# Performance work log

Hardware: AMD Instinct MI355X
Metric: run time of the kernel (lower is better)

The kernel has to match this reference:

```python
import jax, jax.numpy as jnp
import numpy as np

PROJ_DIM = 512
HIDDEN_DIM = 1024
OUTPUT_DIM = 32000
BATCH = 256
TRG_LEN = 512


def setup_inputs() -> dict:
    key = jax.random.key(0)
    ks = jax.random.split(key, 10)
    H = PROJ_DIM
    inp = {
        "x": jax.random.normal(ks[0], (BATCH, TRG_LEN, 1), dtype=jnp.float32),
        "hidden": jnp.zeros((1, BATCH, H), dtype=jnp.float32),
        "trg": jax.random.randint(ks[1], (BATCH, TRG_LEN), 0, OUTPUT_DIM),
        # LSTM params (PyTorch layout, gate order i,f,g,o)
        "w_ih": jax.random.normal(ks[2], (4 * H, 1), dtype=jnp.float32) * (1.0 / np.sqrt(H)),
        "w_hh": jax.random.normal(ks[3], (4 * H, H), dtype=jnp.float32) * (1.0 / np.sqrt(H)),
        "b_ih": jax.random.normal(ks[4], (4 * H,), dtype=jnp.float32) * 0.01,
        "b_hh": jax.random.normal(ks[5], (4 * H,), dtype=jnp.float32) * 0.01,
        "fc1_w": jax.random.normal(ks[6], (HIDDEN_DIM, H), dtype=jnp.float32) * (1.0 / np.sqrt(H)),
        "fc1_b": jnp.zeros((HIDDEN_DIM,), dtype=jnp.float32),
        "fc2_w": jax.random.normal(ks[7], (OUTPUT_DIM, HIDDEN_DIM), dtype=jnp.float32) * (1.0 / np.sqrt(HIDDEN_DIM)),
        "fc2_b": jnp.zeros((OUTPUT_DIM,), dtype=jnp.float32),
    }
    return inp


def reference(x, hidden, trg, w_ih, w_hh, b_ih, b_hh, fc1_w, fc1_b, fc2_w, fc2_b):
    # hidden arg is ignored (source overwrites it with None). Teacher forcing
    # fixed to True: the fed-back argmax never affects LSTM state, and the
    # return value is only the output at the final timestep.
    B, T = trg.shape
    H = w_hh.shape[1]
    bias = b_ih + b_hh  # (4H,)
    # inputs fed at steps t=1..T-1 are trg[:, 0..T-2] as float scalars
    inputs = trg[:, : T - 1].astype(jnp.float32).T[..., None]  # (T-1, B, 1)

    def step(carry, x_t):
        h, c = carry  # (B, H) each
        gates = x_t @ w_ih.T + h @ w_hh.T + bias  # (B, 4H)
        i, f, g, o = jnp.split(gates, 4, axis=-1)
        i = jax.nn.sigmoid(i)
        f = jax.nn.sigmoid(f)
        g = jnp.tanh(g)
        o = jax.nn.sigmoid(o)
        c = f * c + i * g
        h = o * jnp.tanh(c)
        return (h, c), None

    h0 = jnp.zeros((B, H), dtype=jnp.float32)
    c0 = jnp.zeros((B, H), dtype=jnp.float32)
    (h_last, _), _ = jax.lax.scan(step, (h0, c0), inputs)

    # head applied to final timestep's LSTM output: fc2(relu(fc1(h)))
    z = jax.nn.relu(h_last @ fc1_w.T + fc1_b)  # (B, hidden_dim)
    out = z @ fc2_w.T + fc2_b  # (B, output_dim)
    return out
```

## Files before the change

kernel.cpp:

```cpp
#include <hip/hip_runtime.h>
#include <stdint.h>

typedef uint32_t u32;
typedef uint16_t u16;
typedef __attribute__((ext_vector_type(8))) short bf16x8;
typedef __attribute__((ext_vector_type(4))) float f32x4;

__device__ __forceinline__ u16 f2bf(float f) {
  u32 u = __builtin_bit_cast(u32, f);
  return (u16)((u + 0x7FFFu + ((u >> 16) & 1u)) >> 16);
}
__device__ __forceinline__ u32 pack2bf(float a, float b) {
  return (u32)f2bf(a) | ((u32)f2bf(b) << 16);
}
__device__ __forceinline__ uint4 pack8bf(float4 a, float4 b) {
  uint4 r;
  r.x = pack2bf(a.x, a.y); r.y = pack2bf(a.z, a.w);
  r.z = pack2bf(b.x, b.y); r.w = pack2bf(b.z, b.w);
  return r;
}
__device__ __forceinline__ float sigmoid_(float x) { return 1.0f / (1.0f + __expf(-x)); }
__device__ __forceinline__ float tanh_(float x) { return 1.0f - 2.0f / (1.0f + __expf(2.0f * x)); }

__device__ __forceinline__ void store_h_l3(u16* p, u32 v) {
  asm volatile("global_store_short %0, %1, off sc0 sc1" :: "v"(p), "v"(v) : "memory");
}
__device__ __forceinline__ u32 load_flag_l3(const int* p) {
  u32 v;
  asm volatile("global_load_dword %0, %1, off sc0 sc1\n\ts_waitcnt vmcnt(0)"
               : "=v"(v) : "v"(p) : "memory");
  return v;
}

__global__ __launch_bounds__(256, 2) void lstm_kernel(
    const int* __restrict__ trg, const float* __restrict__ w_ih,
    const float* __restrict__ w_hh, const float* __restrict__ b_ih,
    const float* __restrict__ b_hh, u16* __restrict__ h_buf,
    int* __restrict__ flags) {
  __shared__ u16 Bb[16 * 520];
  __shared__ float Xl[16 * 513];
  const int tid = threadIdx.x;
  const int wave = tid >> 6, lane = tid & 63;
  const int q = lane >> 4, n = lane & 15;
  const int bg = blockIdx.x & 15, ug = blockIdx.x >> 4;

  #pragma unroll
  for (int c = 0; c < 4; ++c) {
    int e = c * 2048 + tid * 8;
    int rn = e >> 9, t0 = e & 511;
    const int* src = trg + (bg * 16 + rn) * 512 + t0;
    int4 a = *(const int4*)src;
    int4 b = *(const int4*)(src + 4);
    float* dst = &Xl[rn * 513 + t0];
    dst[0] = (float)a.x; dst[1] = (float)a.y; dst[2] = (float)a.z; dst[3] = (float)a.w;
    dst[4] = (float)b.x; dst[5] = (float)b.y; dst[6] = (float)b.z; dst[7] = (float)b.w;
  }

  bf16x8 Areg[2][16];
  const int rit = lane & 15;
  #pragma unroll
  for (int i = 0; i < 2; ++i) {
    int tile = wave * 2 + i;
    int grow = (rit & 3) * 512 + ug * 32 + tile * 4 + (rit >> 2);
    const float* wr = w_hh + (size_t)grow * 512;
    #pragma unroll
    for (int ks = 0; ks < 16; ++ks) {
      const float* p = wr + ks * 32 + q * 8;
      float4 f0 = *(const float4*)p;
      float4 f1 = *(const float4*)(p + 4);
      Areg[i][ks] = __builtin_bit_cast(bf16x8, pack8bf(f0, f1));
    }
  }

  float wi[2][4], bs[2][4];
  #pragma unroll
  for (int i = 0; i < 2; ++i) {
    int tile = wave * 2 + i;
    #pragma unroll
    for (int r = 0; r < 4; ++r) {
      int grow = r * 512 + ug * 32 + tile * 4 + q;
      wi[i][r] = w_ih[grow];
      bs[i][r] = b_ih[grow] + b_hh[grow];
    }
  }
  float cst[2] = {0.f, 0.f};
  __syncthreads();

  for (int t = 1; t <= 511; ++t) {
    if (t > 1) {
      const int* fp = &flags[(t - 1) * 16 + bg];
      int cnt = 0;
      u32 v;
      do {
        v = load_flag_l3(fp);
        if (++cnt > (1 << 20)) break;
      } while (v < 16u);
    }
    {
      const u16* src = h_buf + (size_t)(((t - 1) & 1) * 16 + bg) * 8192;
      const u16* p0 = src + 0 * 2048 + tid * 8;
      const u16* p1 = src + 1 * 2048 + tid * 8;
      const u16* p2 = src + 2 * 2048 + tid * 8;
      const u16* p3 = src + 3 * 2048 + tid * 8;
      uint4 d0, d1, d2, d3;
      asm volatile(
          "global_load_dwordx4 %0, %4, off sc0 sc1\n\t"
          "global_load_dwordx4 %1, %5, off sc0 sc1\n\t"
          "global_load_dwordx4 %2, %6, off sc0 sc1\n\t"
          "global_load_dwordx4 %3, %7, off sc0 sc1\n\t"
          "s_waitcnt vmcnt(0)"
          : "=&v"(d0), "=&v"(d1), "=&v"(d2), "=&v"(d3)
          : "v"(p0), "v"(p1), "v"(p2), "v"(p3)
          : "memory");
      #pragma unroll
      for (int c = 0; c < 4; ++c) {
        int e = c * 2048 + tid * 8;
        int rn = e >> 9, k = e & 511;
        uint4 d = (c == 0) ? d0 : (c == 1) ? d1 : (c == 2) ? d2 : d3;
        *(uint4*)&Bb[rn * 520 + k] = d;
      }
    }
    __syncthreads();

    f32x4 acc[2] = {{0.f, 0.f, 0.f, 0.f}, {0.f, 0.f, 0.f, 0.f}};
    const u16* brow = &Bb[n * 520];
    #pragma unroll
    for (int ks = 0; ks < 16; ++ks) {
      bf16x8 bf = *(const bf16x8*)(brow + ks * 32 + q * 8);
      acc[0] = __builtin_amdgcn_mfma_f32_16x16x32_bf16(Areg[0][ks], bf, acc[0], 0, 0, 0);
      acc[1] = __builtin_amdgcn_mfma_f32_16x16x32_bf16(Areg[1][ks], bf, acc[1], 0, 0, 0);
    }

    float x = Xl[n * 513 + (t - 1)];
    u16* hdst = h_buf + (size_t)((t & 1) * 16 + bg) * 8192 + n * 512 + ug * 32 + q;
    #pragma unroll
    for (int i = 0; i < 2; ++i) {
      int tile = wave * 2 + i;
      float pi = acc[i][0] + x * wi[i][0] + bs[i][0];
      float pf = acc[i][1] + x * wi[i][1] + bs[i][1];
      float pg = acc[i][2] + x * wi[i][2] + bs[i][2];
      float po = acc[i][3] + x * wi[i][3] + bs[i][3];
      float ig = sigmoid_(pi), fg = sigmoid_(pf), og = sigmoid_(po);
      float gg = tanh_(pg);
      cst[i] = fg * cst[i] + ig * gg;
      float h = og * tanh_(cst[i]);
      store_h_l3(hdst + tile * 4, (u32)f2bf(h));
    }
    asm volatile("s_waitcnt vmcnt(0)" ::: "memory");
    __syncthreads();
    if (tid == 0) {
      __hip_atomic_fetch_add(&flags[t * 16 + bg], 1, __ATOMIC_RELAXED,
                             __HIP_MEMORY_SCOPE_AGENT);
    }
  }
}

__global__ __launch_bounds__(256, 1) void head_gemm(
    const float* __restrict__ A, const u16* __restrict__ B,
    const float* __restrict__ bias, void* __restrict__ outv,
    int M, int K, int mode) {
  __shared__ u16 Ach[128 * 40];
  __shared__ u16 Bch[256 * 40];
  const int tid = threadIdx.x;
  const int wave = tid >> 6, lane = tid & 63;
  const int q = lane >> 4, l15 = lane & 15;
  const int mblk = blockIdx.x * 128;
  const int nch = K >> 5;
  f32x4 acc[2][16];
  #pragma unroll
  for (int i = 0; i < 2; ++i)
    #pragma unroll
    for (int nb = 0; nb < 16; ++nb) acc[i][nb] = (f32x4){0.f, 0.f, 0.f, 0.f};

  for (int ch = 0; ch < nch; ++ch) {
    __syncthreads();
    {
      int row = tid >> 1, k = (tid & 1) * 16;
      const float* src = A + (size_t)(mblk + row) * K + ch * 32 + k;
      float4 f0 = *(const float4*)src;
      float4 f1 = *(const float4*)(src + 4);
      float4 f2 = *(const float4*)(src + 8);
      float4 f3 = *(const float4*)(src + 12);
      u16* dst = &Ach[row * 40 + k];
      *(uint4*)dst = pack8bf(f0, f1);
      *(uint4*)(dst + 8) = pack8bf(f2, f3);
    }
    #pragma unroll
    for (int c = 0; c < 4; ++c) {
      int e = c * 2048 + tid * 8;
      int nr = e >> 5, k = e & 31;
      uint4 d = *(const uint4*)(B + (size_t)nr * K + ch * 32 + k);
      *(uint4*)&Bch[nr * 40 + k] = d;
    }
    __syncthreads();
    bf16x8 a0 = *(const bf16x8*)&Ach[((wave * 2 + 0) * 16 + l15) * 40 + q * 8];
    bf16x8 a1 = *(const bf16x8*)&Ach[((wave * 2 + 1) * 16 + l15) * 40 + q * 8];
    #pragma unroll
    for (int nb = 0; nb < 16; ++nb) {
      bf16x8 bf = *(const bf16x8*)&Bch[(nb * 16 + l15) * 40 + q * 8];
      acc[0][nb] = __builtin_amdgcn_mfma_f32_16x16x32_bf16(a0, bf, acc[0][nb], 0, 0, 0);
      acc[1][nb] = __builtin_amdgcn_mfma_f32_16x16x32_bf16(a1, bf, acc[1][nb], 0, 0, 0);
    }
  }
  #pragma unroll
  for (int i = 0; i < 2; ++i) {
    int j0 = mblk + (wave * 2 + i) * 16 + q * 4;
    float4 bv = *(const float4*)(bias + j0);
    #pragma unroll
    for (int nb = 0; nb < 16; ++nb) {
      int b = nb * 16 + l15;
      f32x4 v = acc[i][nb];
      v[0] += bv.x; v[1] += bv.y; v[2] += bv.z; v[3] += bv.w;
      if (mode == 0) {
        v[0] = fmaxf(v[0], 0.f); v[1] = fmaxf(v[1], 0.f);
        v[2] = fmaxf(v[2], 0.f); v[3] = fmaxf(v[3], 0.f);
        u16* z = (u16*)outv;
        uint2 pk;
        pk.x = pack2bf(v[0], v[1]);
        pk.y = pack2bf(v[2], v[3]);
        *(uint2*)(z + (size_t)b * M + j0) = pk;
      } else {
        float* op = (float*)outv + (size_t)b * M + j0;
        float4 o;
        o.x = v[0]; o.y = v[1]; o.z = v[2]; o.w = v[3];
        *(float4*)op = o;
      }
    }
  }
}

extern "C" void kernel_launch(void* const* d_in, const int* in_sizes, int n_in,
                              void* d_out, int out_size, void* d_ws, size_t ws_size,
                              hipStream_t stream) {
  (void)in_sizes; (void)n_in; (void)out_size; (void)ws_size;
  const int* trg = (const int*)d_in[2];
  const float* w_ih = (const float*)d_in[3];
  const float* w_hh = (const float*)d_in[4];
  const float* b_ih = (const float*)d_in[5];
  const float* b_hh = (const float*)d_in[6];
  const float* fc1_w = (const float*)d_in[7];
  const float* fc1_b = (const float*)d_in[8];
  const float* fc2_w = (const float*)d_in[9];
  const float* fc2_b = (const float*)d_in[10];

  u16* h_buf = (u16*)d_ws;
  int* flags = (int*)((char*)d_ws + 524288);
  u16* z = (u16*)((char*)d_ws + 557056);

  hipMemsetAsync(d_ws, 0, 262144, stream);
  hipMemsetAsync((char*)d_ws + 524288, 0, 32768, stream);

  lstm_kernel<<<256, 256, 0, stream>>>(trg, w_ih, w_hh, b_ih, b_hh, h_buf, flags);

  const u16* h_final = h_buf + 16 * 16 * 512;
  head_gemm<<<8, 256, 0, stream>>>(fc1_w, h_final, fc1_b, (void*)z, 1024, 512, 0);
  head_gemm<<<250, 256, 0, stream>>>(fc2_w, z, fc2_b, d_out, 32000, 1024, 1);
}
```

Before: 1.726 ms.

## Coalesce h stores via LDS and poll flags from a single thread

```diff
diff --git a/kernel.cpp b/kernel.cpp
--- a/kernel.cpp
+++ b/kernel.cpp
@@ -21,16 +21,6 @@
 }
 __device__ __forceinline__ float sigmoid_(float x) { return 1.0f / (1.0f + __expf(-x)); }
 __device__ __forceinline__ float tanh_(float x) { return 1.0f - 2.0f / (1.0f + __expf(2.0f * x)); }
-
-__device__ __forceinline__ void store_h_l3(u16* p, u32 v) {
-  asm volatile("global_store_short %0, %1, off sc0 sc1" :: "v"(p), "v"(v) : "memory");
-}
-__device__ __forceinline__ u32 load_flag_l3(const int* p) {
-  u32 v;
-  asm volatile("global_load_dword %0, %1, off sc0 sc1\n\ts_waitcnt vmcnt(0)"
-               : "=v"(v) : "v"(p) : "memory");
-  return v;
-}
 
 __global__ __launch_bounds__(256, 2) void lstm_kernel(
     const int* __restrict__ trg, const float* __restrict__ w_ih,
@@ -39,6 +29,7 @@
     int* __restrict__ flags) {
   __shared__ u16 Bb[16 * 520];
   __shared__ float Xl[16 * 513];
+  __shared__ u32 Hs[256];
   const int tid = threadIdx.x;
   const int wave = tid >> 6, lane = tid & 63;
   const int q = lane >> 4, n = lane & 15;
@@ -60,8 +51,7 @@
   const int rit = lane & 15;
   #pragma unroll
   for (int i = 0; i < 2; ++i) {
-    int tile = wave * 2 + i;
-    int grow = (rit & 3) * 512 + ug * 32 + tile * 4 + (rit >> 2);
+    int grow = (rit & 3) * 512 + ug * 32 + wave * 8 + 2 * (rit >> 2) + i;
     const float* wr = w_hh + (size_t)grow * 512;
     #pragma unroll
     for (int ks = 0; ks < 16; ++ks) {
@@ -75,10 +65,9 @@
   float wi[2][4], bs[2][4];
   #pragma unroll
   for (int i = 0; i < 2; ++i) {
-    int tile = wave * 2 + i;
     #pragma unroll
     for (int r = 0; r < 4; ++r) {
-      int grow = r * 512 + ug * 32 + tile * 4 + q;
+      int grow = r * 512 + ug * 32 + wave * 8 + q * 2 + i;
       wi[i][r] = w_ih[grow];
       bs[i][r] = b_ih[grow] + b_hh[grow];
     }
@@ -88,13 +77,14 @@
 
   for (int t = 1; t <= 511; ++t) {
     if (t > 1) {
-      const int* fp = &flags[(t - 1) * 16 + bg];
-      int cnt = 0;
-      u32 v;
-      do {
-        v = load_flag_l3(fp);
-        if (++cnt > (1 << 20)) break;
-      } while (v < 16u);
+      if (tid == 0) {
+        int cnt = 0;
+        while (__hip_atomic_load(&flags[(t - 1) * 16 + bg], __ATOMIC_RELAXED,
+                                 __HIP_MEMORY_SCOPE_AGENT) < 16) {
+          if (++cnt > (1 << 22)) break;
+        }
+      }
+      __syncthreads();
     }
     {
       const u16* src = h_buf + (size_t)(((t - 1) & 1) * 16 + bg) * 8192;
@@ -132,10 +122,9 @@
     }
 
     float x = Xl[n * 513 + (t - 1)];
-    u16* hdst = h_buf + (size_t)((t & 1) * 16 + bg) * 8192 + n * 512 + ug * 32 + q;
+    float hv0, hv1;
     #pragma unroll
     for (int i = 0; i < 2; ++i) {
-      int tile = wave * 2 + i;
       float pi = acc[i][0] + x * wi[i][0] + bs[i][0];
       float pf = acc[i][1] + x * wi[i][1] + bs[i][1];
       float pg = acc[i][2] + x * wi[i][2] + bs[i][2];
@@ -144,9 +133,18 @@
       float gg = tanh_(pg);
       cst[i] = fg * cst[i] + ig * gg;
       float h = og * tanh_(cst[i]);
-      store_h_l3(hdst + tile * 4, (u32)f2bf(h));
-    }
-    asm volatile("s_waitcnt vmcnt(0)" ::: "memory");
+      if (i == 0) hv0 = h; else hv1 = h;
+    }
+
+    Hs[n * 16 + wave * 4 + q] = pack2bf(hv0, hv1);
+    __syncthreads();
+    {
+      u32 hv = Hs[tid];
+      u32* dst = (u32*)h_buf + (size_t)((t & 1) ? 65536 : 0) +
+                 (size_t)(bg * 16 + (tid >> 4)) * 256 + ug * 16 + (tid & 15);
+      asm volatile("global_store_dword %0, %1, off sc0 sc1\n\ts_waitcnt vmcnt(0)"
+                   :: "v"(dst), "v"(hv) : "memory");
+    }
     __syncthreads();
     if (tid == 0) {
       __hip_atomic_fetch_add(&flags[t * 16 + bg], 1, __ATOMIC_RELAXED,
@@ -252,7 +250,7 @@
 
   lstm_kernel<<<256, 256, 0, stream>>>(trg, w_ih, w_hh, b_ih, b_hh, h_buf, flags);
 
-  const u16* h_final = h_buf + 16 * 16 * 512;
+  const u16* h_final = h_buf + 131072;
   head_gemm<<<8, 256, 0, stream>>>(fc1_w, h_final, fc1_b, (void*)z, 1024, 512, 0);
   head_gemm<<<250, 256, 0, stream>>>(fc2_w, z, fc2_b, d_out, 32000, 1024, 1);
 }
```

Result: faster. 1.642 ms (-4.8%).
